# Kernel optimization log

Measured on AMD Instinct MI355X. Metric: run time of the kernel, lower is better.

Reference implementation:

```python
import jax, jax.numpy as jnp
from jax import lax
import numpy as np

B, T, C = 8, 4096, 1024


def setup_inputs() -> dict:
    key = jax.random.key(0)
    ks = jax.random.split(key, 10)
    return {
        "x": jax.random.normal(ks[0], (B, T, C), jnp.float32),
        "time_decay": jax.random.uniform(ks[1], (C,), jnp.float32, -6.0, -3.0),
        "time_first": jax.random.normal(ks[2], (C,), jnp.float32) * 0.1 + 1.0,
        "time_mix_k": jax.random.uniform(ks[3], (1, 1, C), jnp.float32),
        "time_mix_v": jax.random.uniform(ks[4], (1, 1, C), jnp.float32),
        "time_mix_r": jax.random.uniform(ks[5], (1, 1, C), jnp.float32),
        "Wk": jax.random.normal(ks[6], (C, C), jnp.float32) * 0.02,
        "Wv": jax.random.normal(ks[7], (C, C), jnp.float32) * 0.02,
        "Wr": jax.random.normal(ks[8], (C, C), jnp.float32) * 0.02,
        "Wo": jax.random.normal(ks[9], (C, C), jnp.float32) * 0.02,
    }


def _wkv_scan(k, v, w, u, pp0):
    # k, v: [B, T, C]; w, u: [C]; pp0: [B, C]
    b, t, c = k.shape
    zeros = jnp.zeros((b, c), jnp.float32)

    def step(carry, kv):
        aa, bb, pp = carry
        kt, vt = kv
        ww = u + pp
        p = jnp.maximum(ww, kt)
        e1 = jnp.exp(ww - p)
        e2 = jnp.exp(kt - p)
        y = (aa * e1 + vt * e2) / (bb * e1 + e2 + 1e-6)
        ww2 = w + pp
        p2 = jnp.maximum(ww2, kt)
        e1b = jnp.exp(ww2 - p2)
        e2b = jnp.exp(kt - p2)
        return (aa * e1b + vt * e2b, bb * e1b + e2b, p2), y

    kT = jnp.swapaxes(k, 0, 1)  # [T, B, C]
    vT = jnp.swapaxes(v, 0, 1)
    _, yT = lax.scan(step, (zeros, zeros, pp0), (kT, vT))
    return jnp.swapaxes(yT, 0, 1)  # [B, T, C]


def reference(x, time_decay, time_first, time_mix_k, time_mix_v, time_mix_r, Wk, Wv, Wr, Wo):
    b, t, c = x.shape
    # time-shift: prepend zero token, drop last
    xx = jnp.concatenate([jnp.zeros((b, 1, c), x.dtype), x[:, :-1]], axis=1)
    xk = x * time_mix_k + xx * (1.0 - time_mix_k)
    xv = x * time_mix_v + xx * (1.0 - time_mix_v)
    xr = x * time_mix_r + xx * (1.0 - time_mix_r)
    k = xk @ Wk.T
    v = xv @ Wv.T
    r = jax.nn.sigmoid(xr @ Wr.T)
    w = -jnp.exp(time_decay)
    u = time_first
    pp0 = jnp.full((b, c), -1e30, jnp.float32)
    y = _wkv_scan(k, v, w, u, pp0)
    return (r * y) @ Wo.T
```

## Files before the change

### kernel.cpp

```cpp
#include <hip/hip_runtime.h>
#include <cstdint>

#define DEV __device__ __forceinline__

constexpr int Bz = 8, Tz = 4096, Cz = 1024;
constexpr int Mz = Bz * Tz;
constexpr int Sz = 32, Lz = 128;

using bf16x8  = __attribute__((ext_vector_type(8))) __bf16;
using floatx4 = __attribute__((ext_vector_type(4))) float;

DEV float bf2f(unsigned short u) { return __uint_as_float(((uint32_t)u) << 16); }
DEV unsigned short f2bf(float f) {
    uint32_t u = __float_as_uint(f);
    u += 0x7fffu + ((u >> 16) & 1u);
    return (unsigned short)(u >> 16);
}
DEV unsigned short f2h(float f) {
    _Float16 h = (_Float16)f;
    unsigned short u;
    __builtin_memcpy(&u, &h, 2);
    return u;
}
DEV float h2f(unsigned short u) {
    _Float16 h;
    __builtin_memcpy(&h, &u, 2);
    return (float)h;
}

DEV void gl2lds16(const unsigned short* g, unsigned short* l) {
    __builtin_amdgcn_global_load_lds(
        (const __attribute__((address_space(1))) void*)g,
        (__attribute__((address_space(3))) void*)l, 16, 0, 0);
}

DEV void barmem() {
    asm volatile("" ::: "memory");
    __builtin_amdgcn_s_barrier();
    asm volatile("" ::: "memory");
}

DEV bf16x8 ldfrag(const unsigned short* slot, int row, int kg) {
    return *(const bf16x8*)&slot[row * 64 + ((kg ^ (row & 7)) << 3)];
}

__global__ __launch_bounds__(256) void f2b_k(const float* __restrict__ w0,
                                             const float* __restrict__ w1,
                                             const float* __restrict__ w2,
                                             const float* __restrict__ w3,
                                             unsigned short* __restrict__ dst) {
    int which = blockIdx.y;
    const float* src = which == 0 ? w0 : which == 1 ? w1 : which == 2 ? w2 : w3;
    int i = blockIdx.x * 256 + threadIdx.x;
    float4 v = ((const float4*)src)[i];
    ushort4 o;
    o.x = f2bf(v.x); o.y = f2bf(v.y); o.z = f2bf(v.z); o.w = f2bf(v.w);
    ((ushort4*)(dst + (size_t)which * Cz * Cz))[i] = o;
}

DEV ushort4 mix4(float4 m, float4 xc, float4 xp) {
    ushort4 o;
    o.x = f2bf(fmaf(m.x, xc.x - xp.x, xp.x));
    o.y = f2bf(fmaf(m.y, xc.y - xp.y, xp.y));
    o.z = f2bf(fmaf(m.z, xc.z - xp.z, xp.z));
    o.w = f2bf(fmaf(m.w, xc.w - xp.w, xp.w));
    return o;
}

__global__ __launch_bounds__(256) void mix_k(const float* __restrict__ x,
    const float* __restrict__ mk, const float* __restrict__ mv, const float* __restrict__ mr,
    unsigned short* __restrict__ xk, unsigned short* __restrict__ xv,
    unsigned short* __restrict__ xr) {
    int gid = blockIdx.x * 256 + threadIdx.x;
    int m   = gid >> 8;
    int c4  = gid & 255;
    float4 xc = ((const float4*)x)[gid];
    float4 xp = make_float4(0.f, 0.f, 0.f, 0.f);
    if ((m & (Tz - 1)) != 0) xp = ((const float4*)x)[gid - 256];
    ((ushort4*)xk)[gid] = mix4(((const float4*)mk)[c4], xc, xp);
    ((ushort4*)xv)[gid] = mix4(((const float4*)mv)[c4], xc, xp);
    ((ushort4*)xr)[gid] = mix4(((const float4*)mr)[c4], xc, xp);
}

__global__ __launch_bounds__(512, 2) void gemm256(
        const unsigned short* __restrict__ A0, const unsigned short* __restrict__ A1,
        const unsigned short* __restrict__ A2,
        const unsigned short* __restrict__ Bw0, const unsigned short* __restrict__ Bw1,
        const unsigned short* __restrict__ Bw2,
        void* __restrict__ O0, void* __restrict__ O1, void* __restrict__ O2,
        int modes) {
    constexpr int Kd = 1024, Nd = 1024, NT = 16;
    __shared__ __align__(16) unsigned short lds[8 * 8192];

    const int cpx = gridDim.x >> 3;
    const int L   = (blockIdx.x & 7) * cpx + (blockIdx.x >> 3);
    const int z   = L >> 9;
    const int rr  = L & 511;
    const int m0  = (rr >> 2) << 8;
    const int n0  = (rr & 3) << 8;

    const unsigned short* A  = z == 0 ? A0  : z == 1 ? A1  : A2;
    const unsigned short* Bw = z == 0 ? Bw0 : z == 1 ? Bw1 : Bw2;
    void* Cout = z == 0 ? O0 : z == 1 ? O1 : O2;
    const int mode = (modes >> (z * 4)) & 15;

    const int tid  = threadIdx.x;
    const int lane = tid & 63;
    const int wave = tid >> 6;
    const int wr   = wave >> 2;
    const int wc   = wave & 3;
    const int l15  = lane & 15, kseg = lane >> 4;
    const int brow = (wc & 1) * 64;

    const int g0   = wave * 128 + lane;
    const int row0 = g0 >> 3;
    const int scg0 = (g0 & 7) ^ (row0 & 7);
    const size_t soff0 = (size_t)row0 * Kd + scg0 * 8;
    const int sd0  = g0 * 8;

    auto STAGE = [&](int hh) {
        if (hh >= 4 * NT) return;
        const int kind = hh & 3;
        const unsigned short* mat = (kind & 2) ? Bw : A;
        const int rbase = ((kind & 2) ? n0 : m0) + ((kind & 1) << 7);
        const unsigned short* sb = mat + (size_t)rbase * Kd + ((hh >> 2) << 6);
        unsigned short* db = &lds[(hh & 7) * 8192];
        gl2lds16(sb + soff0,            db + sd0);
        gl2lds16(sb + soff0 + 8 * Kd,   db + sd0 + 512);
    };

    floatx4 acc[8][4];
#pragma unroll
    for (int mi = 0; mi < 8; mi++)
#pragma unroll
        for (int ni = 0; ni < 4; ni++) acc[mi][ni] = (floatx4){0.f, 0.f, 0.f, 0.f};

    auto QUAD = [&](const bf16x8 (&af)[4], const bf16x8 (&bfv)[4], int mo) {
#pragma unroll
        for (int i = 0; i < 4; i++)
#pragma unroll
            for (int n = 0; n < 4; n++)
                acc[mo + i][n] = __builtin_amdgcn_mfma_f32_16x16x32_bf16(
                    af[i], bfv[n], acc[mo + i][n], 0, 0, 0);
    };

#pragma unroll
    for (int hh = 0; hh < 6; hh++) STAGE(hh);
    asm volatile("s_waitcnt vmcnt(4)" ::: "memory");
    barmem();

#pragma unroll 2
    for (int t = 0; t < NT; t++) {
        const unsigned short* sA = &lds[(((t & 1) << 2) + wr) * 8192];
        const unsigned short* sB = &lds[(((t & 1) << 2) + 2 + (wc >> 1)) * 8192];
        const int bh = 4 * t + 6;
        bf16x8 a00[4], a01[4], a10[4], a11[4], b0[4], b1[4];

#pragma unroll
        for (int i = 0; i < 4; i++) {
            int ra = i * 16 + l15;
            a00[i] = ldfrag(sA, ra, kseg);
            a01[i] = ldfrag(sA, ra, 4 + kseg);
            b0[i]  = ldfrag(sB, brow + i * 16 + l15, kseg);
        }
        STAGE(bh + 0);
        barmem();
        asm volatile("s_waitcnt lgkmcnt(4)" ::: "memory");
        __builtin_amdgcn_s_setprio(1);
        QUAD(a00, b0, 0);
        __builtin_amdgcn_s_setprio(0);
        barmem();

#pragma unroll
        for (int i = 0; i < 4; i++) {
            int ra = 64 + i * 16 + l15;
            a10[i] = ldfrag(sA, ra, kseg);
            a11[i] = ldfrag(sA, ra, 4 + kseg);
        }
        STAGE(bh + 1);
        barmem();
        asm volatile("s_waitcnt lgkmcnt(0)" ::: "memory");
        __builtin_amdgcn_s_setprio(1);
        QUAD(a10, b0, 4);
        __builtin_amdgcn_s_setprio(0);
        barmem();

#pragma unroll
        for (int i = 0; i < 4; i++)
            b1[i] = ldfrag(sB, brow + i * 16 + l15, 4 + kseg);
        STAGE(bh + 2);
        barmem();
        asm volatile("s_waitcnt lgkmcnt(0)" ::: "memory");
        __builtin_amdgcn_s_setprio(1);
        QUAD(a01, b1, 0);
        __builtin_amdgcn_s_setprio(0);
        barmem();

        STAGE(bh + 3);
        barmem();
        __builtin_amdgcn_s_setprio(1);
        QUAD(a11, b1, 4);
        __builtin_amdgcn_s_setprio(0);
        if (t < NT - 2) asm volatile("s_waitcnt vmcnt(4)" ::: "memory");
        else            asm volatile("s_waitcnt vmcnt(0)" ::: "memory");
        barmem();
    }

    const int cr = kseg * 4;
#pragma unroll
    for (int mi = 0; mi < 8; mi++) {
#pragma unroll
        for (int ni = 0; ni < 4; ni++) {
            size_t row = (size_t)(m0 + wr * 128 + mi * 16 + cr);
            size_t col = (size_t)(n0 + wc * 64 + ni * 16 + l15);
#pragma unroll
            for (int rg = 0; rg < 4; rg++) {
                float v = acc[mi][ni][rg];
                size_t idx = (row + rg) * Nd + col;
                if (mode == 0) {
                    ((float*)Cout)[idx] = v;
                } else if (mode == 1) {
                    ((unsigned short*)Cout)[idx] = f2bf(v);
                } else if (mode == 2) {
                    float sg = 1.0f / (1.0f + __expf(-v));
                    ((unsigned short*)Cout)[idx] = f2bf(sg);
                } else {
                    ((unsigned short*)Cout)[idx] = f2h(v);
                }
            }
        }
    }
}

__global__ __launch_bounds__(256) void wkv_pass1(const unsigned short* __restrict__ kh,
    const unsigned short* __restrict__ vb, const float* __restrict__ td,
    float2* __restrict__ SA, float2* __restrict__ SB) {
    int tid = blockIdx.x * 256 + threadIdx.x;
    int c2  = tid & 511;
    int bs  = tid >> 9;
    int b   = bs >> 5, s = bs & (Sz - 1);
    int c   = c2 * 2;
    float lam0 = __expf(-__expf(td[c]));
    float lam1 = __expf(-__expf(td[c + 1]));
    size_t base = (((size_t)(b * Tz + s * Lz)) * Cz + c) >> 1;
    float pa0 = 0.f, pb0 = 0.f, pa1 = 0.f, pb1 = 0.f;
#pragma unroll 4
    for (int i = 0; i < Lz; i++) {
        size_t idx = base + (size_t)i * (Cz / 2);
        ushort2 kk = ((const ushort2*)kh)[idx];
        ushort2 vv = ((const ushort2*)vb)[idx];
        float e0 = __expf(h2f(kk.x)), e1 = __expf(h2f(kk.y));
        pa0 = fmaf(pa0, lam0, e0 * bf2f(vv.x));
        pb0 = fmaf(pb0, lam0, e0);
        pa1 = fmaf(pa1, lam1, e1 * bf2f(vv.y));
        pb1 = fmaf(pb1, lam1, e1);
    }
    SA[tid] = make_float2(pa0, pa1);
    SB[tid] = make_float2(pb0, pb1);
}

__global__ __launch_bounds__(256) void wkv_pass2(const float* __restrict__ td,
                                                 float2* __restrict__ SA,
                                                 float2* __restrict__ SB) {
    int tid = blockIdx.x * 256 + threadIdx.x;
    int c2  = tid & 511;
    int b   = tid >> 9;
    int c   = c2 * 2;
    float lamL0 = __expf(-__expf(td[c]) * (float)Lz);
    float lamL1 = __expf(-__expf(td[c + 1]) * (float)Lz);
    float A0 = 0.f, B0 = 0.f, A1 = 0.f, B1 = 0.f;
    for (int s = 0; s < Sz; s++) {
        size_t idx = ((size_t)(b * Sz + s)) * 512 + c2;
        float2 ta = SA[idx], tb = SB[idx];
        SA[idx] = make_float2(A0, A1);
        SB[idx] = make_float2(B0, B1);
        A0 = fmaf(A0, lamL0, ta.x);  B0 = fmaf(B0, lamL0, tb.x);
        A1 = fmaf(A1, lamL1, ta.y);  B1 = fmaf(B1, lamL1, tb.y);
    }
}

__global__ __launch_bounds__(256) void wkv_pass3(const unsigned short* __restrict__ kh,
    const unsigned short* __restrict__ vb, const unsigned short* __restrict__ rb,
    const float* __restrict__ td, const float* __restrict__ tf,
    const float2* __restrict__ SA, const float2* __restrict__ SB,
    unsigned short* __restrict__ ry) {
    int tid = blockIdx.x * 256 + threadIdx.x;
    int c2  = tid & 511;
    int bs  = tid >> 9;
    int b   = bs >> 5, s = bs & (Sz - 1);
    int c   = c2 * 2;
    float lam0 = __expf(-__expf(td[c]));
    float lam1 = __expf(-__expf(td[c + 1]));
    float eu0  = __expf(tf[c]);
    float eu1  = __expf(tf[c + 1]);
    float2 fa = SA[tid], fb = SB[tid];
    float A0 = fa.x, A1 = fa.y, B0 = fb.x, B1 = fb.y;
    size_t base = (((size_t)(b * Tz + s * Lz)) * Cz + c) >> 1;
#pragma unroll 2
    for (int i = 0; i < Lz; i++) {
        size_t idx = base + (size_t)i * (Cz / 2);
        ushort2 kk = ((const ushort2*)kh)[idx];
        ushort2 vv = ((const ushort2*)vb)[idx];
        ushort2 rr = ((const ushort2*)rb)[idx];
        float e0 = __expf(h2f(kk.x)), e1 = __expf(h2f(kk.y));
        float ev0 = e0 * bf2f(vv.x), ev1 = e1 * bf2f(vv.y);
        float y0 = fmaf(A0, eu0, ev0) * __builtin_amdgcn_rcpf(fmaf(B0, eu0, e0));
        float y1 = fmaf(A1, eu1, ev1) * __builtin_amdgcn_rcpf(fmaf(B1, eu1, e1));
        ushort2 o;
        o.x = f2bf(bf2f(rr.x) * y0);
        o.y = f2bf(bf2f(rr.y) * y1);
        ((ushort2*)ry)[idx] = o;
        A0 = fmaf(A0, lam0, ev0);  B0 = fmaf(B0, lam0, e0);
        A1 = fmaf(A1, lam1, ev1);  B1 = fmaf(B1, lam1, e1);
    }
}

extern "C" void kernel_launch(void* const* d_in, const int* in_sizes, int n_in,
                              void* d_out, int out_size, void* d_ws, size_t ws_size,
                              hipStream_t stream) {
    const float* x  = (const float*)d_in[0];
    const float* td = (const float*)d_in[1];
    const float* tf = (const float*)d_in[2];
    const float* mk = (const float*)d_in[3];
    const float* mv = (const float*)d_in[4];
    const float* mr = (const float*)d_in[5];
    const float* Wk = (const float*)d_in[6];
    const float* Wv = (const float*)d_in[7];
    const float* Wr = (const float*)d_in[8];
    const float* Wo = (const float*)d_in[9];

    constexpr size_t SZ_BF = (size_t)Mz * Cz * 2;
    constexpr size_t SZ_W  = (size_t)Cz * Cz * 2;
    constexpr size_t SZ_S  = (size_t)Bz * Sz * Cz * 4;

    char* ws = (char*)d_ws;
    unsigned short* xk  = (unsigned short*)(ws);
    unsigned short* xv  = (unsigned short*)(ws + SZ_BF);
    unsigned short* xr  = (unsigned short*)(ws + 2 * SZ_BF);
    unsigned short* kf  = (unsigned short*)(ws + 3 * SZ_BF);
    unsigned short* vb  = (unsigned short*)(ws + 4 * SZ_BF);
    unsigned short* rb  = (unsigned short*)(ws + 5 * SZ_BF);
    unsigned short* wts = (unsigned short*)(ws + 6 * SZ_BF);
    float2*         SA  = (float2*)        (ws + 6 * SZ_BF + 4 * SZ_W);
    float2*         SB  = (float2*)        (ws + 6 * SZ_BF + 4 * SZ_W + SZ_S);
    unsigned short* wkb = wts;
    unsigned short* wvb = wts + (size_t)Cz * Cz;
    unsigned short* wrb = wts + (size_t)2 * Cz * Cz;
    unsigned short* wob = wts + (size_t)3 * Cz * Cz;
    unsigned short* ry  = xk;

    f2b_k<<<dim3(Cz * Cz / 4 / 256, 4), dim3(256), 0, stream>>>(Wk, Wv, Wr, Wo, wts);

    mix_k<<<dim3(Mz * Cz / 4 / 256), dim3(256), 0, stream>>>(x, mk, mv, mr, xk, xv, xr);

    gemm256<<<dim3(512 * 3), dim3(512), 0, stream>>>(
        xk, xv, xr, wkb, wvb, wrb, (void*)kf, (void*)vb, (void*)rb,
        (3) | (1 << 4) | (2 << 8));

    wkv_pass1<<<dim3(Bz * Sz * Cz / 2 / 256), dim3(256), 0, stream>>>(kf, vb, td, SA, SB);
    wkv_pass2<<<dim3(Bz * Cz / 2 / 256), dim3(256), 0, stream>>>(td, SA, SB);
    wkv_pass3<<<dim3(Bz * Sz * Cz / 2 / 256), dim3(256), 0, stream>>>(kf, vb, rb, td, tf,
                                                                      SA, SB, ry);

    gemm256<<<dim3(512), dim3(512), 0, stream>>>(
        ry, ry, ry, wob, wob, wob, d_out, d_out, d_out, 0);
}
```

Before: 706.9 us.

## Restructure GEMM LDS staging into half-K slabs with new swizzle and pipeline

The LDS layout changes from per-128-row blocks with 64-wide K and XOR-by-row swizzle to full-256-row slabs split into two 32-wide K halves, using a new swizzle keyed on row pairs. The main loop is rewritten as a TILE routine with explicit vmcnt/lgkmcnt waits, sched barriers, and a peeled prologue and epilogue. The aim is fewer LDS bank conflicts and better overlap of global-to-LDS copies with MFMA work. Each wave now reloads B fragments per half rather than keeping a and b fragments for both K halves, which trades register pressure for more LDS reads.

```diff
diff --git a/kernel.cpp b/kernel.cpp
--- a/kernel.cpp
+++ b/kernel.cpp
@@ -38,10 +38,6 @@
     asm volatile("" ::: "memory");
     __builtin_amdgcn_s_barrier();
     asm volatile("" ::: "memory");
-}
-
-DEV bf16x8 ldfrag(const unsigned short* slot, int row, int kg) {
-    return *(const bf16x8*)&slot[row * 64 + ((kg ^ (row & 7)) << 3)];
 }
 
 __global__ __launch_bounds__(256) void f2b_k(const float* __restrict__ w0,
@@ -110,23 +106,25 @@
     const int wr   = wave >> 2;
     const int wc   = wave & 3;
     const int l15  = lane & 15, kseg = lane >> 4;
-    const int brow = (wc & 1) * 64;
-
-    const int g0   = wave * 128 + lane;
-    const int row0 = g0 >> 3;
-    const int scg0 = (g0 & 7) ^ (row0 & 7);
-    const size_t soff0 = (size_t)row0 * Kd + scg0 * 8;
-    const int sd0  = g0 * 8;
-
-    auto STAGE = [&](int hh) {
-        if (hh >= 4 * NT) return;
-        const int kind = hh & 3;
-        const unsigned short* mat = (kind & 2) ? Bw : A;
-        const int rbase = ((kind & 2) ? n0 : m0) + ((kind & 1) << 7);
-        const unsigned short* sb = mat + (size_t)rbase * Kd + ((hh >> 2) << 6);
-        unsigned short* db = &lds[(hh & 7) * 8192];
-        gl2lds16(sb + soff0,            db + sd0);
-        gl2lds16(sb + soff0 + 8 * Kd,   db + sd0 + 512);
+    const int wr128 = wr * 128, wc64 = wc * 64;
+
+    const int gi   = wave * 64 + lane;
+    const int srow = gi >> 2;
+    const int sg   = (gi & 3) ^ ((srow >> 1) & 3);
+    const size_t sofs = (size_t)srow * Kd + sg * 8;
+    const int gi8  = gi * 8;
+
+    auto STAGE = [&](int kind, int tt) {
+        const unsigned short* mat = (kind >= 2) ? Bw : A;
+        const int rb = (kind >= 2) ? n0 : m0;
+        const unsigned short* sb = mat + (size_t)rb * Kd + tt * 64 + (kind & 1) * 32;
+        unsigned short* db = &lds[(((tt & 1) << 2) + kind) * 8192];
+        gl2lds16(sb + sofs,                    db + gi8);
+        gl2lds16(sb + sofs + (size_t)128 * Kd, db + gi8 + 4096);
+    };
+
+    auto LDF = [&](const unsigned short* slot, int row) -> bf16x8 {
+        return *(const bf16x8*)&slot[row * 32 + ((kseg ^ ((row >> 1) & 3)) << 3)];
     };
 
     floatx4 acc[8][4];
@@ -144,75 +142,94 @@
                     af[i], bfv[n], acc[mo + i][n], 0, 0, 0);
     };
 
-#pragma unroll
-    for (int hh = 0; hh < 6; hh++) STAGE(hh);
-    asm volatile("s_waitcnt vmcnt(4)" ::: "memory");
+    auto VMW = [&](int n) {
+        if (n == 8)      { asm volatile("s_waitcnt vmcnt(8)" ::: "memory"); }
+        else if (n == 4) { asm volatile("s_waitcnt vmcnt(4)" ::: "memory"); }
+        else             { asm volatile("s_waitcnt vmcnt(0)" ::: "memory"); }
+        __builtin_amdgcn_sched_barrier(0);
+    };
+    auto LKW = [&]() {
+        asm volatile("s_waitcnt lgkmcnt(0)" ::: "memory");
+        __builtin_amdgcn_sched_barrier(0);
+    };
+
+    auto TILE = [&](int t, bool s01, bool s23, int w1, int w2) {
+        const unsigned short* Ak0 = &lds[((t & 1) << 2) * 8192];
+        const unsigned short* Ak1 = Ak0 + 8192;
+        const unsigned short* Bk0 = Ak0 + 2 * 8192;
+        const unsigned short* Bk1 = Ak0 + 3 * 8192;
+        bf16x8 fa[4], fb[4];
+
+#pragma unroll
+        for (int i = 0; i < 4; i++) {
+            fa[i] = LDF(Ak0, wr128 + i * 16 + l15);
+            fb[i] = LDF(Bk0, wc64 + i * 16 + l15);
+        }
+        if (s01) STAGE(1, t + 1);
+        barmem();
+        LKW();
+        __builtin_amdgcn_s_setprio(1);
+        QUAD(fa, fb, 0);
+        __builtin_amdgcn_s_setprio(0);
+        barmem();
+
+#pragma unroll
+        for (int i = 0; i < 4; i++)
+            fa[i] = LDF(Ak0, wr128 + 64 + i * 16 + l15);
+        if (s01) STAGE(3, t + 1);
+        barmem();
+        LKW();
+        __builtin_amdgcn_s_setprio(1);
+        QUAD(fa, fb, 4);
+        __builtin_amdgcn_s_setprio(0);
+        VMW(w1);
+        barmem();
+
+#pragma unroll
+        for (int i = 0; i < 4; i++) {
+            fa[i] = LDF(Ak1, wr128 + i * 16 + l15);
+            fb[i] = LDF(Bk1, wc64 + i * 16 + l15);
+        }
+        if (s23) STAGE(0, t + 2);
+        barmem();
+        LKW();
+        __builtin_amdgcn_s_setprio(1);
+        QUAD(fa, fb, 0);
+        __builtin_amdgcn_s_setprio(0);
+        barmem();
+
+#pragma unroll
+        for (int i = 0; i < 4; i++)
+            fa[i] = LDF(Ak1, wr128 + 64 + i * 16 + l15);
+        if (s23) STAGE(2, t + 2);
+        barmem();
+        LKW();
+        __builtin_amdgcn_s_setprio(1);
+        QUAD(fa, fb, 4);
+        __builtin_amdgcn_s_setprio(0);
+        if (w2 >= 0) VMW(w2);
+        barmem();
+    };
+
+    STAGE(0, 0); STAGE(2, 0);
+    STAGE(1, 0); STAGE(3, 0);
+    STAGE(0, 1); STAGE(2, 1);
+    VMW(8);
     barmem();
 
 #pragma unroll 2
-    for (int t = 0; t < NT; t++) {
-        const unsigned short* sA = &lds[(((t & 1) << 2) + wr) * 8192];
-        const unsigned short* sB = &lds[(((t & 1) << 2) + 2 + (wc >> 1)) * 8192];
-        const int bh = 4 * t + 6;
-        bf16x8 a00[4], a01[4], a10[4], a11[4], b0[4], b1[4];
-
-#pragma unroll
-        for (int i = 0; i < 4; i++) {
-            int ra = i * 16 + l15;
-            a00[i] = ldfrag(sA, ra, kseg);
-            a01[i] = ldfrag(sA, ra, 4 + kseg);
-            b0[i]  = ldfrag(sB, brow + i * 16 + l15, kseg);
-        }
-        STAGE(bh + 0);
-        barmem();
-        asm volatile("s_waitcnt lgkmcnt(4)" ::: "memory");
-        __builtin_amdgcn_s_setprio(1);
-        QUAD(a00, b0, 0);
-        __builtin_amdgcn_s_setprio(0);
-        barmem();
-
-#pragma unroll
-        for (int i = 0; i < 4; i++) {
-            int ra = 64 + i * 16 + l15;
-            a10[i] = ldfrag(sA, ra, kseg);
-            a11[i] = ldfrag(sA, ra, 4 + kseg);
-        }
-        STAGE(bh + 1);
-        barmem();
-        asm volatile("s_waitcnt lgkmcnt(0)" ::: "memory");
-        __builtin_amdgcn_s_setprio(1);
-        QUAD(a10, b0, 4);
-        __builtin_amdgcn_s_setprio(0);
-        barmem();
-
-#pragma unroll
-        for (int i = 0; i < 4; i++)
-            b1[i] = ldfrag(sB, brow + i * 16 + l15, 4 + kseg);
-        STAGE(bh + 2);
-        barmem();
-        asm volatile("s_waitcnt lgkmcnt(0)" ::: "memory");
-        __builtin_amdgcn_s_setprio(1);
-        QUAD(a01, b1, 0);
-        __builtin_amdgcn_s_setprio(0);
-        barmem();
-
-        STAGE(bh + 3);
-        barmem();
-        __builtin_amdgcn_s_setprio(1);
-        QUAD(a11, b1, 4);
-        __builtin_amdgcn_s_setprio(0);
-        if (t < NT - 2) asm volatile("s_waitcnt vmcnt(4)" ::: "memory");
-        else            asm volatile("s_waitcnt vmcnt(0)" ::: "memory");
-        barmem();
-    }
+    for (int t = 0; t < NT - 2; t++)
+        TILE(t, true, true, 8, 8);
+    TILE(NT - 2, true, false, 8, 4);
+    TILE(NT - 1, false, false, 0, -1);
 
     const int cr = kseg * 4;
 #pragma unroll
     for (int mi = 0; mi < 8; mi++) {
 #pragma unroll
         for (int ni = 0; ni < 4; ni++) {
-            size_t row = (size_t)(m0 + wr * 128 + mi * 16 + cr);
-            size_t col = (size_t)(n0 + wc * 64 + ni * 16 + l15);
+            size_t row = (size_t)(m0 + wr128 + mi * 16 + cr);
+            size_t col = (size_t)(n0 + wc64 + ni * 16 + l15);
 #pragma unroll
             for (int rg = 0; rg < 4; rg++) {
                 float v = acc[mi][ni][rg];
@@ -222,8 +239,8 @@
                 } else if (mode == 1) {
                     ((unsigned short*)Cout)[idx] = f2bf(v);
                 } else if (mode == 2) {
-                    float sg = 1.0f / (1.0f + __expf(-v));
-                    ((unsigned short*)Cout)[idx] = f2bf(sg);
+                    float sg2 = 1.0f / (1.0f + __expf(-v));
+                    ((unsigned short*)Cout)[idx] = f2bf(sg2);
                 } else {
                     ((unsigned short*)Cout)[idx] = f2h(v);
                 }
```

Result: no change. 703.2 us (-0.5%).
